# Performance work log

Hardware: AMD Instinct MI355X
Metric: run time of the kernel (lower is better)

The kernel has to match this reference:

```python
import jax, jax.numpy as jnp
import numpy as np

# Fixed production-scale dims (see shape_source)
B, R, WIDTH, T, H, W = 8, 12, 2304, 4, 16, 29
REDUCE, HID, NC, ROI_SP, DEPTH = 1024, 512, 60, 7, 2
SR = 2  # roi_align sampling ratio (fixed; torchvision default -1 is roi-adaptive)


def conv2d(x, w, pad):
    return jax.lax.conv_general_dilated(
        x, w, (1, 1), [(pad, pad), (pad, pad)],
        dimension_numbers=('NCHW', 'OIHW', 'NCHW'))


def maxpool_3x3_s2(x):
    return jax.lax.reduce_window(
        x, -jnp.inf, jax.lax.max, (1, 1, 3, 3), (1, 1, 2, 2),
        [(0, 0), (0, 0), (1, 1), (1, 1)])


def bilinear(img, ys, xs):
    # img [C,h,w]; ys, xs [P] -> [C,P]; matches torchvision bilinear_interpolate
    h, w = img.shape[1], img.shape[2]
    valid = (ys >= -1.0) & (ys <= h) & (xs >= -1.0) & (xs <= w)
    y = jnp.clip(ys, 0.0, h - 1.0)
    x = jnp.clip(xs, 0.0, w - 1.0)
    y0f = jnp.floor(y); x0f = jnp.floor(x)
    iy0 = y0f.astype(jnp.int32); ix0 = x0f.astype(jnp.int32)
    iy1 = jnp.minimum(iy0 + 1, h - 1); ix1 = jnp.minimum(ix0 + 1, w - 1)
    ly = y - y0f; lx = x - x0f; hy = 1.0 - ly; hx = 1.0 - lx
    v00 = img[:, iy0, ix0]; v01 = img[:, iy0, ix1]
    v10 = img[:, iy1, ix0]; v11 = img[:, iy1, ix1]
    out = hy * hx * v00 + hy * lx * v01 + ly * hx * v10 + ly * lx * v11
    return jnp.where(valid[None, :], out, 0.0)


def roi_align_one(img, box):
    # img [C,H,W]; box (x1,y1,x2,y2) in feature coords; aligned=False, scale=1
    x1, y1, x2, y2 = box[0], box[1], box[2], box[3]
    rw = jnp.maximum(x2 - x1, 1.0)
    rh = jnp.maximum(y2 - y1, 1.0)
    bw = rw / ROI_SP; bh = rh / ROI_SP
    g = (jnp.arange(ROI_SP, dtype=jnp.float32)[:, None]
         + (jnp.arange(SR, dtype=jnp.float32)[None, :] + 0.5) / SR).reshape(-1)  # [7*SR]
    ys = y1 + g * bh; xs = x1 + g * bw
    n = ROI_SP * SR
    yy = jnp.repeat(ys, n); xx = jnp.tile(xs, n)
    vals = bilinear(img, yy, xx)                       # [C, n*n]
    vals = vals.reshape(img.shape[0], ROI_SP, SR, ROI_SP, SR)
    return vals.mean(axis=(2, 4))                      # [C,7,7]


def hr2o_layer(x, qw, kw, vw, cw, gamma, beta):
    # x [R, HID, Hp, Wp]; non-local attention across ROIs of one image
    q = conv2d(x, qw, 1)
    k = conv2d(x, kw, 1)
    v = conv2d(x, vw, 1)
    att = jnp.einsum('ichw,jchw->ijhw', q, k) / jnp.sqrt(jnp.float32(HID))
    att = jax.nn.softmax(att, axis=1)                  # softmax over key rois
    virt = jnp.einsum('ijhw,jchw->ichw', att, v)
    mu = virt.mean(axis=(1, 2, 3), keepdims=True)      # GroupNorm(1, HID)
    var = virt.var(axis=(1, 2, 3), keepdims=True)
    virt = (virt - mu) / jnp.sqrt(var + 1e-5)
    virt = virt * gamma[None, :, None, None] + beta[None, :, None, None]
    virt = jax.nn.relu(virt)
    virt = conv2d(virt, cw, 1)                         # mlp_1x1=False -> 3x3 pad 1
    return x + virt                                    # dropout inactive in eval


def setup_inputs() -> dict:
    key = jax.random.key(0)
    ks = jax.random.split(key, 14)
    features = jax.random.normal(ks[0], (B, WIDTH, T, H, W), jnp.float32)
    xy = jax.random.uniform(ks[1], (B, R, 2), minval=0.0, maxval=0.6)
    wh = jax.random.uniform(ks[2], (B, R, 2), minval=0.2, maxval=0.4)
    rois = jnp.concatenate([xy, xy + wh], axis=-1)     # normalized x1,y1,x2,y2

    def w_(k, shape, fan_in):
        return jax.random.normal(k, shape, jnp.float32) * (1.0 / np.sqrt(fan_in))

    return {
        'features': features,
        'rois': rois,
        'conv_reduce_w': w_(ks[3], (REDUCE, WIDTH, 1, 1), WIDTH),
        'conv1_w': w_(ks[4], (HID, 2 * REDUCE, 1, 1), 2 * REDUCE),
        'conv2_w': w_(ks[5], (HID, HID, 3, 3), HID * 9),
        'hr2o_qw': w_(ks[6], (DEPTH, HID, HID, 3, 3), HID * 9),
        'hr2o_kw': w_(ks[7], (DEPTH, HID, HID, 3, 3), HID * 9),
        'hr2o_vw': w_(ks[8], (DEPTH, HID, HID, 3, 3), HID * 9),
        'hr2o_cw': w_(ks[9], (DEPTH, HID, HID, 3, 3), HID * 9),
        'hr2o_gamma': jnp.ones((DEPTH, HID), jnp.float32),
        'hr2o_beta': jnp.zeros((DEPTH, HID), jnp.float32),
        'fc1_w': w_(ks[10], (HID, REDUCE), REDUCE),
        'fc2_w': w_(ks[11], (NC, 2 * HID), 2 * HID),
    }


def reference(features, rois, conv_reduce_w, conv1_w, conv2_w,
              hr2o_qw, hr2o_kw, hr2o_vw, hr2o_cw, hr2o_gamma, hr2o_beta,
              fc1_w, fc2_w):
    feats = features.mean(axis=2)                      # AdaptiveAvgPool3d((1,H,W)) over T
    feats = conv2d(feats, conv_reduce_w, 0)            # [B, REDUCE, H, W]

    scale = jnp.array([W, H, W, H], jnp.float32)
    boxes = rois * scale                               # feature-space coords (detached)
    ra = jax.vmap(lambda img, bxs: jax.vmap(lambda b: roi_align_one(img, b))(bxs))(
        feats, boxes)                                  # [B, R, REDUCE, 7, 7]
    roi_feats = ra.max(axis=(-2, -1)).reshape(B * R, REDUCE)  # MaxPool2d(7)

    # broadcast bg + tiled actor, concat on channels (eff_h=H, eff_w=W)
    bg = jnp.broadcast_to(feats[:, None], (B, R, REDUCE, H, W))
    actor = jnp.broadcast_to(
        roi_feats.reshape(B, R, REDUCE)[..., None, None], (B, R, REDUCE, H, W))
    x = jnp.concatenate([bg, actor], axis=2).reshape(B * R, 2 * REDUCE, H, W)
    x = jax.nn.relu(conv2d(x, conv1_w, 0))             # 1x1
    x = jax.nn.relu(conv2d(x, conv2_w, 0))             # 3x3, Conv2d default pad=0
    x = maxpool_3x3_s2(x)                              # [B*R, HID, 7, 14]
    hp, wp = x.shape[2], x.shape[3]
    x = x.reshape(B, R, HID, hp, wp)
    for d in range(DEPTH):
        x = jax.vmap(lambda xi: hr2o_layer(
            xi, hr2o_qw[d], hr2o_kw[d], hr2o_vw[d], hr2o_cw[d],
            hr2o_gamma[d], hr2o_beta[d]))(x)
    high = x.mean(axis=(-2, -1)).reshape(B * R, HID)   # GAP

    out = jax.nn.relu(roi_feats @ fc1_w.T)
    out = jnp.concatenate([out, high], axis=1)
    return out @ fc2_w.T                               # [B*R, NC]
```

## Files before the change

kernel.cpp:

```cpp
#include <hip/hip_runtime.h>
#include <math.h>

#define BB 8
#define RR 12
#define WIDTH 2304
#define TT 4
#define HH 16
#define WW 29
#define HWIN (HH*WW)
#define REDUCE 1024
#define HID 512
#define NC 60
#define DEPTH 2
#define NIMG (BB*RR)
#define OH2 14
#define OW2 27
#define NSP2 (OH2*OW2)
#define PH 7
#define PW 14
#define NSP (PH*PW)
#define ATT_SCALE 0.044194173824159216f

typedef __attribute__((ext_vector_type(8))) short short8;
typedef __attribute__((ext_vector_type(4))) float floatx4;

__device__ __forceinline__ void split2(float v, unsigned short& h, unsigned short& l)
{
    union { float f; unsigned u; } c; c.f = v;
    unsigned hb = c.u & 0xffff0000u;
    h = (unsigned short)(hb >> 16);
    union { float f; unsigned u; } hc; hc.u = hb;
    float r = v - hc.f;
    union { float f; unsigned u; } rc; rc.f = r;
    unsigned ru = rc.u + 0x7fffu + ((rc.u >> 16) & 1u);
    l = (unsigned short)(ru >> 16);
}

__device__ __forceinline__ void gll16(const void* g, void* l)
{
    __builtin_amdgcn_global_load_lds((const __attribute__((address_space(1))) void*)g,
                                     (__attribute__((address_space(3))) void*)l,
                                     16, 0, 0);
}

#define MFMA3(d, ah_, al_, bh_, bl_) \
    d = __builtin_amdgcn_mfma_f32_16x16x32_bf16(ah_, bh_, d, 0, 0, 0); \
    d = __builtin_amdgcn_mfma_f32_16x16x32_bf16(ah_, bl_, d, 0, 0, 0); \
    d = __builtin_amdgcn_mfma_f32_16x16x32_bf16(al_, bh_, d, 0, 0, 0);

template<int TYPE, int NSEL, bool RELU, bool RESID, int WR, int ZB>
__global__ __launch_bounds__(256, 2)
void tapr_k(const int4* __restrict__ WA0, const int4* __restrict__ WA1, const int4* __restrict__ WA2,
            const ushort* __restrict__ BH, const ushort* __restrict__ BL,
            const float* __restrict__ Res,
            float* __restrict__ Y0, float* __restrict__ Y1, float* __restrict__ Y2)
{
    __shared__ int4 L[2064 + ZB * 8 * WR];
    const int tid = threadIdx.x;
    constexpr int NZP = 96 / ZB;

    int ch, zp, nb = 0;
    if (TYPE == 0) { ch = blockIdx.x / NZP; zp = blockIdx.x % NZP; }
    else { ch = blockIdx.x / (4 * NZP); int r = blockIdx.x % (4 * NZP); nb = r / NZP; zp = r % NZP; }
    int sel = 0, m0;
    if (NSEL == 3) { sel = ch >> 2; m0 = (ch & 3) * 128; }
    else m0 = ch * 128;
    const int z0 = zp * ZB;

    const int4* WA = (NSEL == 3) ? (sel == 0 ? WA0 : sel == 1 ? WA1 : WA2) : WA0;
    float* Y = (NSEL == 3) ? (sel == 0 ? Y0 : sel == 1 ? Y1 : Y2) : Y0;

    const int lane = tid & 63, wv = tid >> 6;
    const int lrow = lane >> 4, lcol = lane & 15;
    constexpr long ALO = 294912;
    constexpr long PLSTR = (TYPE == 1) ? 472L * 512 : 160L * 512;
    const int pbase = (TYPE == 1) ? (((nb * 112) >> 5) * 29 + ((nb * 112) & 31)) : 0;

    int pbnf[7];
#pragma unroll
    for (int nf = 0; nf < 7; ++nf) {
        int col = nf * 16 + lcol;
        if (TYPE == 0) pbnf[nf] = col;
        else { int gn = nb * 112 + col; pbnf[nf] = (gn >> 5) * 29 + (gn & 31) - pbase; }
    }

    int uR[3], uPl[3], uZi[3]; bool uV[3];
    const ushort* uSrc[3];
#pragma unroll
    for (int it = 0; it < 3; ++it) {
        int u = tid + it * 256;
        uV[it] = (u < 2 * ZB * WR);
        int uu = uV[it] ? u : 0;
        uR[it] = uu % WR; uPl[it] = (uu / WR) & 1; uZi[it] = uu / (2 * WR);
        const ushort* P = uPl[it] ? BL : BH;
        uSrc[it] = P + (size_t)(z0 + uZi[it]) * PLSTR + (size_t)(pbase + uR[it]) * 512;
    }

    floatx4 acc[ZB][2][7];
#pragma unroll
    for (int zi = 0; zi < ZB; ++zi)
#pragma unroll
        for (int mf = 0; mf < 2; ++mf)
#pragma unroll
            for (int nf = 0; nf < 7; ++nf) acc[zi][mf][nf] = (floatx4){0.f, 0.f, 0.f, 0.f};

#define BCOPY(CB) { \
    _Pragma("unroll") \
    for (int it = 0; it < 3; ++it) if (uV[it]) { \
        const int4* s = (const int4*)(uSrc[it] + (size_t)(CB) * 32); \
        int4 t0 = s[0], t1 = s[1], t2 = s[2], t3_ = s[3]; \
        int bse = 2064 + uZi[it] * (8 * WR) + uPl[it] * (4 * WR) + uR[it]; \
        L[bse] = t0; L[bse + WR] = t1; L[bse + 2 * WR] = t2; L[bse + 3 * WR] = t3_; \
    } }

#define ASTAGE(KST, BUF) { \
    int k8 = (KST) * 4; \
    _Pragma("unroll") \
    for (int j = 0; j < 4; ++j) { \
        int h = wv * 4 + j, p = h >> 3, g = (h >> 1) & 3, hf = h & 1; \
        gll16(WA + (p ? ALO : 0) + (long)(k8 + g) * 512 + m0 + hf * 64 + lane, \
              L + (BUF) * 1032 + (p * 4 + g) * 129 + hf * 64); \
    } }

#define COMPUTE(BUF, SHV) { \
    const int4* La = L + (BUF) * 1032; \
    short8 ah[2], al[2]; \
    _Pragma("unroll") \
    for (int mf = 0; mf < 2; ++mf) { \
        int au = lrow * 129 + (wv * 2 + mf) * 16 + lcol; \
        ah[mf] = *(const short8*)(La + au); \
        al[mf] = *(const short8*)(La + 516 + au); \
    } \
    _Pragma("unroll") \
    for (int nf = 0; nf < 7; ++nf) { \
        int spl = pbnf[nf] + (SHV); \
        _Pragma("unroll") \
        for (int zi = 0; zi < ZB; ++zi) { \
            const int4* Lb = L + 2064 + zi * (8 * WR) + lrow * WR + spl; \
            short8 bh = *(const short8*)(Lb); \
            short8 bl = *(const short8*)(Lb + 4 * WR); \
            _Pragma("unroll") \
            for (int mf = 0; mf < 2; ++mf) { MFMA3(acc[zi][mf][nf], ah[mf], al[mf], bh, bl) } \
        } \
    } }

    BCOPY(0)
    ASTAGE(0, 0)
    __syncthreads();

    int cur = 0;
    for (int cb = 0; cb < 16; ++cb) {
#pragma unroll
        for (int tap = 0; tap < 9; ++tap) {
            const int kst = cb * 9 + tap;
            const int t3 = tap / 3;
            const int shv = (TYPE == 0) ? (t3 * 16 + (tap - t3 * 3)) : (t3 * 29 + (tap - t3 * 3));
            if (kst < 143) ASTAGE(kst + 1, cur ^ 1)
            COMPUTE(cur, shv)
            __syncthreads();
            cur ^= 1;
        }
        if (cb < 15) {
            BCOPY(cb + 1)
            __syncthreads();
        }
    }

#pragma unroll
    for (int zi = 0; zi < ZB; ++zi) {
        const int z = z0 + zi;
#pragma unroll
        for (int mf = 0; mf < 2; ++mf) {
            int m = m0 + wv * 32 + mf * 16 + lrow * 4;
#pragma unroll
            for (int nf = 0; nf < 7; ++nf) {
                int col = nf * 16 + lcol;
                int sp, realn; bool ok;
                if (TYPE == 0) { int oh = col >> 4, ow = col & 15; ok = ow < 14; sp = oh * 14 + ow; realn = 98; }
                else { int gn = nb * 112 + col; int oh = gn >> 5, ow = gn & 31; ok = ow < 27; sp = oh * 27 + ow; realn = 378; }
                if (ok) {
#pragma unroll
                    for (int r = 0; r < 4; ++r) {
                        size_t idx = ((size_t)z * 512 + m + r) * realn + sp;
                        float v = acc[zi][mf][nf][r];
                        if (RESID) v += Res[idx];
                        if (RELU) v = fmaxf(v, 0.f);
                        Y[idx] = v;
                    }
                }
            }
        }
    }
#undef BCOPY
#undef ASTAGE
#undef COMPUTE
}

template<int KW, int KSTN, int MTOT, long PLSTR, int NREAL>
__global__ __launch_bounds__(256, 2)
void tapc_k(const int4* __restrict__ WA,
            const ushort* __restrict__ BH, const ushort* __restrict__ BL,
            float* __restrict__ Y)
{
    __shared__ int4 L[3872];
    const int tid = threadIdx.x;
    const int z = blockIdx.z, nb = blockIdx.x;
    const int m0 = blockIdx.y * 128;
    const int lane = tid & 63, wv = tid >> 6;
    const int lrow = lane >> 4, lcol = lane & 15;
    constexpr long ALO = (long)KSTN * 4 * MTOT;

    int nU[2], gU[2]; long pbU[2]; bool vU[2];
#pragma unroll
    for (int it = 0; it < 2; ++it) {
        int u = tid + (it << 8);
        vU[it] = (u < 448);
        int uu = vU[it] ? u : 0;
        nU[it] = uu % 112; gU[it] = uu / 112;
        int gn = nb * 112 + nU[it];
        pbU[it] = min(gn, NREAL - 1);
    }
    const ushort* BHz = BH + (size_t)z * PLSTR;
    const ushort* BLz = BL + (size_t)z * PLSTR;

    floatx4 acc[2][7];
#pragma unroll
    for (int mf = 0; mf < 2; ++mf)
#pragma unroll
        for (int nf = 0; nf < 7; ++nf) acc[mf][nf] = (floatx4){0.f, 0.f, 0.f, 0.f};

    short8 rbh[2], rbl[2];

#define STAGE_ISSUE(KST, BUF) { \
    int k8 = (KST) * 4; \
    _Pragma("unroll") \
    for (int j = 0; j < 4; ++j) { \
        int h = wv * 4 + j, p = h >> 3, g = (h >> 1) & 3, hf = h & 1; \
        gll16(WA + (p ? ALO : 0) + (long)(k8 + g) * MTOT + m0 + hf * 64 + lane, \
              L + (BUF) * 1936 + (p * 4 + g) * 129 + hf * 64); \
    } \
    int ci0 = (KST) << 5; \
    _Pragma("unroll") \
    for (int it = 0; it < 2; ++it) if (vU[it]) { \
        size_t o = (size_t)pbU[it] * KW + ci0 + gU[it] * 8; \
        rbh[it] = *(const short8*)(BHz + o); \
        rbl[it] = *(const short8*)(BLz + o); \
    } }

#define STAGE_WRITE(BUF) { \
    _Pragma("unroll") \
    for (int it = 0; it < 2; ++it) if (vU[it]) { \
        *((short8*)(L + (BUF) * 1936 + 1032 + gU[it] * 113 + nU[it])) = rbh[it]; \
        *((short8*)(L + (BUF) * 1936 + 1484 + gU[it] * 113 + nU[it])) = rbl[it]; \
    } }

#define COMPUTE(BUF) { \
    const int4* Lc = L + (BUF) * 1936; \
    short8 ah[2], al[2]; \
    _Pragma("unroll") \
    for (int mf = 0; mf < 2; ++mf) { \
        int au = lrow * 129 + (wv * 2 + mf) * 16 + lcol; \
        ah[mf] = *(const short8*)(Lc + au); \
        al[mf] = *(const short8*)(Lc + 516 + au); \
    } \
    _Pragma("unroll") \
    for (int nf = 0; nf < 7; ++nf) { \
        int bu = 1032 + lrow * 113 + nf * 16 + lcol; \
        short8 bh = *(const short8*)(Lc + bu); \
        short8 bl = *(const short8*)(Lc + bu + 452); \
        _Pragma("unroll") \
        for (int mf = 0; mf < 2; ++mf) { MFMA3(acc[mf][nf], ah[mf], al[mf], bh, bl) } \
    } }

    STAGE_ISSUE(0, 0)
    STAGE_WRITE(0)
    __syncthreads();

    int cur = 0;
    for (int kst = 0; kst < KSTN; ++kst) {
        int nxt = cur ^ 1;
        bool more = (kst + 1 < KSTN);
        if (more) STAGE_ISSUE(kst + 1, nxt)
        COMPUTE(cur)
        if (more) { STAGE_WRITE(nxt) __syncthreads(); }
        cur = nxt;
    }

#pragma unroll
    for (int mf = 0; mf < 2; ++mf) {
        int m = m0 + wv * 32 + mf * 16 + lrow * 4;
#pragma unroll
        for (int nf = 0; nf < 7; ++nf) {
            int col = nf * 16 + lcol;
            int gn = nb * 112 + col;
            if (gn < NREAL) {
#pragma unroll
                for (int r = 0; r < 4; ++r) {
                    size_t idx = ((size_t)z * MTOT + m + r) * NREAL + gn;
                    Y[idx] = acc[mf][nf][r];
                }
            }
        }
    }
#undef STAGE_ISSUE
#undef STAGE_WRITE
#undef COMPUTE
}

__global__ void prep_w_k(const float* __restrict__ s0, const float* __restrict__ s1,
                         const float* __restrict__ s2, const float* __restrict__ s3,
                         int4* __restrict__ dst)
{
    const int c = blockIdx.y;
    const float* src = (c == 0) ? s0 : (c == 1) ? s1 : (c == 2) ? s2 : s3;
    int4* dh = dst + (size_t)c * 589824;
    int4* dl = dh + 294912;
    int idx = blockIdx.x * 256 + threadIdx.x;
    if (idx >= 294912) return;
    int g8 = idx / 512, m = idx & 511;
    unsigned hw[4], lw[4];
#pragma unroll
    for (int j = 0; j < 4; ++j) {
        int k1 = g8 * 8 + 2 * j, k2 = k1 + 1;
        int cb1 = k1 / 288, r1 = k1 % 288, tp1 = r1 >> 5, ci1 = cb1 * 32 + (r1 & 31);
        int cb2 = k2 / 288, r2 = k2 % 288, tp2 = r2 >> 5, ci2 = cb2 * 32 + (r2 & 31);
        float v1 = src[(size_t)m * 4608 + ci1 * 9 + tp1];
        float v2 = src[(size_t)m * 4608 + ci2 * 9 + tp2];
        unsigned short h0, l0, h1, l1;
        split2(v1, h0, l0); split2(v2, h1, l1);
        hw[j] = (unsigned)h0 | ((unsigned)h1 << 16);
        lw[j] = (unsigned)l0 | ((unsigned)l1 << 16);
    }
    dh[idx] = make_int4(hw[0], hw[1], hw[2], hw[3]);
    dl[idx] = make_int4(lw[0], lw[1], lw[2], lw[3]);
}

__global__ void prep_wg_k(const float* __restrict__ src, int ldw, int M, int K8,
                          int4* __restrict__ dst)
{
    int idx = blockIdx.x * 256 + threadIdx.x;
    if (idx >= K8 * M) return;
    int g8 = idx / M, m = idx % M;
    unsigned hw[4], lw[4];
#pragma unroll
    for (int j = 0; j < 4; ++j) {
        int k1 = g8 * 8 + 2 * j;
        float v1 = src[(size_t)m * ldw + k1];
        float v2 = src[(size_t)m * ldw + k1 + 1];
        unsigned short h0, l0, h1, l1;
        split2(v1, h0, l0); split2(v2, h1, l1);
        hw[j] = (unsigned)h0 | ((unsigned)h1 << 16);
        lw[j] = (unsigned)l0 | ((unsigned)l1 << 16);
    }
    dst[idx] = make_int4(hw[0], hw[1], hw[2], hw[3]);
    dst[(size_t)K8 * M + idx] = make_int4(lw[0], lw[1], lw[2], lw[3]);
}

__global__ __launch_bounds__(256)
void tsplit_k(const float* __restrict__ src, ushort* __restrict__ dh, ushort* __restrict__ dl,
              int C, int S, long zsrc, long zdst)
{
    __shared__ float t[64][65];
    const int c0 = blockIdx.x * 64, s0 = blockIdx.y * 64, z = blockIdx.z;
    const float* sz = src + (size_t)z * zsrc;
    const int tx = threadIdx.x & 63, ty = threadIdx.x >> 6;
#pragma unroll
    for (int i = 0; i < 16; ++i) {
        int cc = i * 4 + ty;
        int c = c0 + cc, s = s0 + tx;
        t[cc][tx] = (c < C && s < S) ? sz[(size_t)c * S + s] : 0.f;
    }
    __syncthreads();
#pragma unroll
    for (int i = 0; i < 16; ++i) {
        int ss = i * 4 + ty;
        int s = s0 + ss, c = c0 + tx;
        if (s < S && c < C) {
            unsigned short h, l;
            split2(t[tx][ss], h, l);
            size_t o = (size_t)z * zdst + (size_t)s * C + c;
            dh[o] = h; dl[o] = l;
        }
    }
}

__global__ __launch_bounds__(256)
void tsplit_c2_k(const float* __restrict__ bg, const float* __restrict__ bias1,
                 ushort* __restrict__ dh, ushort* __restrict__ dl)
{
    __shared__ float t[64][65];
    const int c0 = blockIdx.x * 64, s0 = blockIdx.y * 64, z = blockIdx.z;
    const int b = z / RR;
    const int tx = threadIdx.x & 63, ty = threadIdx.x >> 6;
#pragma unroll
    for (int i = 0; i < 16; ++i) {
        int cc = i * 4 + ty;
        int s = s0 + tx;
        t[cc][tx] = (s < 464) ? bg[((size_t)b * 512 + c0 + cc) * 464 + s] : 0.f;
    }
    __syncthreads();
    const float bv = bias1[z * 512 + c0 + tx];
#pragma unroll
    for (int i = 0; i < 16; ++i) {
        int ss = i * 4 + ty;
        int s = s0 + ss, c = c0 + tx;
        if (s < 472) {
            float v = (s < 464) ? fmaxf(t[tx][ss] + bv, 0.f) : 0.f;
            unsigned short h, l;
            split2(v, h, l);
            size_t o = (size_t)z * 241664 + (size_t)s * 512 + c;
            dh[o] = h; dl[o] = l;
        }
    }
}

__global__ __launch_bounds__(256)
void tsplit_pad_k(const float* __restrict__ x, ushort* __restrict__ dh, ushort* __restrict__ dl)
{
    __shared__ float t[64 * 99];
    const int c0 = blockIdx.x * 64, z = blockIdx.y;
    const int tid = threadIdx.x;
#pragma unroll
    for (int i = 0; i < 25; ++i) {
        int idx = tid + i * 256;
        if (idx < 6272) {
            int c = idx / 98, s = idx % 98;
            t[c * 99 + s] = x[((size_t)z * 512 + c0 + c) * 98 + s];
        }
    }
    __syncthreads();
#pragma unroll
    for (int i = 0; i < 40; ++i) {
        int idx = tid + i * 256;
        int sp = idx >> 6, c = idx & 63;
        int r = sp >> 4, col = sp & 15;
        float v = (r >= 1 && r <= 7 && col >= 1 && col <= 14) ? t[c * 99 + (r - 1) * 14 + col - 1] : 0.f;
        unsigned short h, l;
        split2(v, h, l);
        size_t o = (size_t)z * 81920 + (size_t)sp * 512 + c0 + c;
        dh[o] = h; dl[o] = l;
    }
}

__global__ void tmean_k(const float* __restrict__ f, float* __restrict__ o, int total)
{
    int i = blockIdx.x * blockDim.x + threadIdx.x;
    if (i >= total) return;
    int p = i % HWIN; long bc = i / HWIN;
    const float* src = f + bc * (long)TT * HWIN + p;
    o[i] = (src[0] + src[HWIN] + src[2 * HWIN] + src[3 * HWIN]) * 0.25f;
}

__global__ __launch_bounds__(256)
void roi_align_k(const float* __restrict__ feats, const float* __restrict__ rois,
                 float* __restrict__ roi_feats)
{
    __shared__ int s_o00[196], s_o01[196], s_o10[196], s_o11[196];
    __shared__ float s_w[4][196];
    const int n = blockIdx.x;
    const int b = n / RR;
    const int t = threadIdx.x;
    if (t < 196) {
        float x1 = rois[n * 4 + 0] * WW, y1 = rois[n * 4 + 1] * HH;
        float x2 = rois[n * 4 + 2] * WW, y2 = rois[n * 4 + 3] * HH;
        float rw = fmaxf(x2 - x1, 1.f), rh = fmaxf(y2 - y1, 1.f);
        float bw = rw / 7.f, bh = rh / 7.f;
        int j = t / 14, i = t % 14;
        float gy = (float)(j >> 1) + ((j & 1) + 0.5f) * 0.5f;
        float gx = (float)(i >> 1) + ((i & 1) + 0.5f) * 0.5f;
        float ys = y1 + gy * bh, xs = x1 + gx * bw;
        bool valid = (ys >= -1.f) && (ys <= (float)HH) && (xs >= -1.f) && (xs <= (float)WW);
        float y = fminf(fmaxf(ys, 0.f), (float)(HH - 1));
        float x = fminf(fmaxf(xs, 0.f), (float)(WW - 1));
        float y0f = floorf(y), x0f = floorf(x);
        int iy0 = (int)y0f, ix0 = (int)x0f;
        int iy1 = min(iy0 + 1, HH - 1), ix1 = min(ix0 + 1, WW - 1);
        float ly = y - y0f, lx = x - x0f, hy = 1.f - ly, hx = 1.f - lx;
        float msk = valid ? 1.f : 0.f;
        s_o00[t] = iy0 * WW + ix0; s_o01[t] = iy0 * WW + ix1;
        s_o10[t] = iy1 * WW + ix0; s_o11[t] = iy1 * WW + ix1;
        s_w[0][t] = hy * hx * msk; s_w[1][t] = hy * lx * msk;
        s_w[2][t] = ly * hx * msk; s_w[3][t] = ly * lx * msk;
    }
    __syncthreads();
    for (int c = t; c < REDUCE; c += 256) {
        const float* img = feats + ((long)(b * REDUCE + c)) * HWIN;
        float mx = -INFINITY;
        for (int bin = 0; bin < 49; ++bin) {
            int by_ = bin / 7, bx = bin % 7;
            float s = 0.f;
#pragma unroll
            for (int sy = 0; sy < 2; ++sy)
#pragma unroll
                for (int sx = 0; sx < 2; ++sx) {
                    int ss = (by_ * 2 + sy) * 14 + bx * 2 + sx;
                    s += s_w[0][ss] * img[s_o00[ss]] + s_w[1][ss] * img[s_o01[ss]]
                       + s_w[2][ss] * img[s_o10[ss]] + s_w[3][ss] * img[s_o11[ss]];
                }
            mx = fmaxf(mx, s * 0.25f);
        }
        roi_feats[(long)n * REDUCE + c] = mx;
    }
}

__global__ void dots_k(const float* __restrict__ Xr, const float* __restrict__ Wt,
                       int ldw, int woff, float* __restrict__ Y,
                       int Nrows, int M, int K, int relu)
{
    int idx = blockIdx.x * blockDim.x + threadIdx.x;
    if (idx >= Nrows * M) return;
    int o = idx / Nrows, n = idx % Nrows;
    const float* xr = Xr + (long)n * K;
    const float* w = Wt + (long)o * ldw + woff;
    float acc = 0.f;
    for (int k = 0; k < K; ++k) acc = fmaf(xr[k], w[k], acc);
    if (relu) acc = fmaxf(acc, 0.f);
    Y[(long)n * M + o] = acc;
}

__global__ void maxpool_k(const float* __restrict__ in, float* __restrict__ out, int total)
{
    int idx = blockIdx.x * blockDim.x + threadIdx.x;
    if (idx >= total) return;
    int ow = idx % PW; int r = idx / PW; int oh = r % PH; long nc = r / PH;
    const float* src = in + nc * NSP2;
    float m = -INFINITY;
    for (int kh = 0; kh < 3; ++kh) {
        int ih = oh * 2 - 1 + kh; if (ih < 0 || ih >= OH2) continue;
        for (int kw = 0; kw < 3; ++kw) {
            int iw = ow * 2 - 1 + kw; if (iw < 0 || iw >= OW2) continue;
            m = fmaxf(m, src[ih * OW2 + iw]);
        }
    }
    out[idx] = m;
}

__global__ __launch_bounds__(256)
void att2_k(const float* __restrict__ q, const float* __restrict__ k, float* __restrict__ att)
{
    __shared__ float qs[5376];
    __shared__ float ks[5376];
    __shared__ float sc[1008];
    const int b = blockIdx.x, p0 = blockIdx.y * 7;
    const int tid = threadIdx.x;

    int itI[4], itJ[4], itP[4]; bool itV[4];
#pragma unroll
    for (int r = 0; r < 4; ++r) {
        int item = tid + (r << 8);
        itV[r] = item < 1008;
        int it = itV[r] ? item : 0;
        int ij = it / 7; itP[r] = it % 7;
        itI[r] = ij / 12; itJ[r] = ij % 12;
    }
    float acc[4] = {0.f, 0.f, 0.f, 0.f};

    for (int cc0 = 0; cc0 < 512; cc0 += 64) {
        for (int l = tid; l < 5376; l += 256) {
            int i = l / 448, r = l % 448, c = r / 7, p = r % 7;
            size_t off = ((size_t)(b * 12 + i) * 512 + cc0 + c) * 98 + p0 + p;
            qs[l] = q[off];
            ks[l] = k[off];
        }
        __syncthreads();
#pragma unroll
        for (int r = 0; r < 4; ++r) {
            if (itV[r]) {
                const float* qp = qs + itI[r] * 448 + itP[r];
                const float* kp = ks + itJ[r] * 448 + itP[r];
                float a = acc[r];
#pragma unroll 8
                for (int c = 0; c < 64; ++c) a = fmaf(qp[c * 7], kp[c * 7], a);
                acc[r] = a;
            }
        }
        __syncthreads();
    }
#pragma unroll
    for (int r = 0; r < 4; ++r)
        if (itV[r]) sc[tid + (r << 8)] = acc[r] * ATT_SCALE;
    __syncthreads();
    if (tid < 84) {
        int i = tid / 7, p = tid % 7;
        float m = -INFINITY;
        float v[12];
#pragma unroll
        for (int j = 0; j < 12; ++j) { v[j] = sc[(i * 12 + j) * 7 + p]; m = fmaxf(m, v[j]); }
        float s = 0.f;
#pragma unroll
        for (int j = 0; j < 12; ++j) { v[j] = expf(v[j] - m); s += v[j]; }
        float inv = 1.f / s;
#pragma unroll
        for (int j = 0; j < 12; ++j)
            att[((size_t)(b * 12 + i) * 12 + j) * 98 + p0 + p] = v[j] * inv;
    }
}

__global__ __launch_bounds__(256)
void virt2_k(const float* __restrict__ att, const float* __restrict__ v, float* __restrict__ virt)
{
    __shared__ float as_[14112];
    const int b = blockIdx.x, cb = blockIdx.y;
    const int tid = threadIdx.x;
    for (int l = tid; l < 14112; l += 256) as_[l] = att[(size_t)b * 14112 + l];
    __syncthreads();

    for (int it = tid; it < 6272; it += 256) {
        int c = cb * 64 + it / 98, p = it % 98;
        float o[12];
#pragma unroll
        for (int i = 0; i < 12; ++i) o[i] = 0.f;
#pragma unroll
        for (int j = 0; j < 12; ++j) {
            float vj = v[((size_t)(b * 12 + j) * 512 + c) * 98 + p];
#pragma unroll
            for (int i = 0; i < 12; ++i) o[i] = fmaf(as_[(i * 12 + j) * 98 + p], vj, o[i]);
        }
#pragma unroll
        for (int i = 0; i < 12; ++i)
            virt[((size_t)(b * 12 + i) * 512 + c) * 98 + p] = o[i];
    }
}

__global__ __launch_bounds__(256)
void stats_k(const float* __restrict__ virt, float* __restrict__ mu, float* __restrict__ rstd)
{
    int n = blockIdx.x;
    const float* src = virt + (long)n * HID * NSP;
    float s = 0.f, q = 0.f;
    for (int i = threadIdx.x; i < HID * NSP; i += 256) {
        float v = src[i]; s += v; q = fmaf(v, v, q);
    }
    for (int off = 32; off; off >>= 1) { s += __shfl_down(s, off); q += __shfl_down(q, off); }
    __shared__ float ss[4], sq[4];
    int w = threadIdx.x >> 6;
    if ((threadIdx.x & 63) == 0) { ss[w] = s; sq[w] = q; }
    __syncthreads();
    if (threadIdx.x == 0) {
        float S = ss[0] + ss[1] + ss[2] + ss[3];
        float Q = sq[0] + sq[1] + sq[2] + sq[3];
        const float invN = 1.f / (HID * NSP);
        float m = S * invN;
        float var = Q * invN - m * m;
        mu[n] = m; rstd[n] = rsqrtf(var + 1e-5f);
    }
}

__global__ void norm_k(float* __restrict__ virt, const float* __restrict__ mu,
                       const float* __restrict__ rstd,
                       const float* __restrict__ gamma, const float* __restrict__ beta)
{
    int idx = blockIdx.x * blockDim.x + threadIdx.x;
    const int TOT = NIMG * HID * NSP;
    if (idx >= TOT) return;
    int n = idx / (HID * NSP);
    int c = (idx / NSP) % HID;
    float val = (virt[idx] - mu[n]) * rstd[n] * gamma[c] + beta[c];
    virt[idx] = fmaxf(val, 0.f);
}

__global__ void meanpool_k(const float* __restrict__ x, float* __restrict__ high)
{
    int idx = blockIdx.x * blockDim.x + threadIdx.x;
    if (idx >= NIMG * HID) return;
    const float* src = x + (long)idx * NSP;
    float s = 0.f;
    for (int p = 0; p < NSP; ++p) s += src[p];
    high[idx] = s * (1.f / NSP);
}

__global__ void final_k(const float* __restrict__ fc1o, const float* __restrict__ high,
                        const float* __restrict__ fc2, float* __restrict__ out)
{
    int idx = blockIdx.x * blockDim.x + threadIdx.x;
    if (idx >= NIMG * NC) return;
    int n = idx / NC, o = idx % NC;
    const float* w = fc2 + (long)o * (2 * HID);
    const float* a = fc1o + (long)n * HID;
    const float* h = high + (long)n * HID;
    float acc = 0.f;
    for (int c = 0; c < HID; ++c) acc = fmaf(a[c], w[c], acc);
    for (int c = 0; c < HID; ++c) acc = fmaf(h[c], w[HID + c], acc);
    out[idx] = acc;
}

extern "C" void kernel_launch(void* const* d_in, const int* in_sizes, int n_in,
                              void* d_out, int out_size, void* d_ws, size_t ws_size,
                              hipStream_t stream)
{
    (void)in_sizes; (void)n_in; (void)out_size; (void)ws_size;
    const float* features = (const float*)d_in[0];
    const float* rois     = (const float*)d_in[1];
    const float* w_reduce = (const float*)d_in[2];
    const float* w_conv1  = (const float*)d_in[3];
    const float* w_conv2  = (const float*)d_in[4];
    const float* qw       = (const float*)d_in[5];
    const float* kw       = (const float*)d_in[6];
    const float* vw       = (const float*)d_in[7];
    const float* cw       = (const float*)d_in[8];
    const float* gamma    = (const float*)d_in[9];
    const float* beta     = (const float*)d_in[10];
    const float* fc1      = (const float*)d_in[11];
    const float* fc2      = (const float*)d_in[12];
    float* ws = (float*)d_ws;

    float*  tmean = ws + 0;
    ushort* tmTH  = (ushort*)(ws + 8552448);
    ushort* tmTL  = (ushort*)(ws + 12828672);
    float*  feats = ws + 17104896;
    ushort* ftTH  = (ushort*)(ws + 0);
    ushort* ftTL  = (ushort*)(ws + 1900544);
    ushort* B2H   = (ushort*)(ws + 0);
    ushort* B2L   = (ushort*)(ws + 11599872);
    int4*   WTQ   = (int4*)(ws + 0);
    float*  bg    = ws + 23199744;
    float*  out2  = ws + 23199744;
    float*  qb    = ws + 23199744;
    float*  kb    = ws + 28016640;
    float*  vb    = ws + 32833536;
    ushort* PTH   = (ushort*)(ws + 41779200);
    ushort* PTL   = (ushort*)(ws + 45711360);
    float*  xb    = ws + 49643520;
    float*  virt  = ws + 54460416;
    int4*   WTS   = (int4*)(ws + 59277312);
    float*  rf    = ws + 61636608;
    float*  bias1 = ws + 61734912;
    float*  fc1o  = ws + 61784064;
    float*  attb  = ws + 61833216;
    float*  mu    = ws + 61946112;
    float*  rstd  = ws + 61946240;
    float*  high  = ws + 61946368;

    dim3 blk(256);

    prep_wg_k<<<1152, blk, 0, stream>>>(w_reduce, 2304, 1024, 288, WTS);

    { int tot = BB * WIDTH * HWIN;
      tmean_k<<<(tot + 255) / 256, blk, 0, stream>>>(features, tmean, tot); }

    tsplit_k<<<dim3(36, 8, 8), blk, 0, stream>>>(tmean, tmTH, tmTL, 2304, 464, 1069056, 1069056);

    tapc_k<2304, 72, 1024, 464L * 2304, 464>
        <<<dim3(5, 8, 8), blk, 0, stream>>>(WTS, tmTH, tmTL, feats);

    tsplit_k<<<dim3(16, 8, 8), blk, 0, stream>>>(feats, ftTH, ftTL, 1024, 464, 475136, 475136);

    roi_align_k<<<96, blk, 0, stream>>>(feats, rois, rf);
    dots_k<<<(NIMG * HID + 255) / 256, blk, 0, stream>>>(rf, w_conv1, 2048, 1024, bias1, NIMG, HID, REDUCE, 0);
    dots_k<<<(NIMG * HID + 255) / 256, blk, 0, stream>>>(rf, fc1, 1024, 0, fc1o, NIMG, HID, REDUCE, 1);

    prep_wg_k<<<256, blk, 0, stream>>>(w_conv1, 2048, 512, 128, WTS);
    tapc_k<1024, 32, 512, 464L * 1024, 464>
        <<<dim3(5, 4, 8), blk, 0, stream>>>(WTS, ftTH, ftTL, bg);

    prep_w_k<<<dim3(1152, 1), blk, 0, stream>>>(w_conv2, w_conv2, w_conv2, w_conv2, WTS);
    tsplit_c2_k<<<dim3(8, 8, 96), blk, 0, stream>>>(bg, bias1, B2H, B2L);

    tapr_k<1, 1, true, false, 165, 2><<<768, blk, 0, stream>>>(
        WTS, nullptr, nullptr, B2H, B2L, nullptr, out2, nullptr, nullptr);

    { int tot = NIMG * HID * NSP;
      maxpool_k<<<(tot + 255) / 256, blk, 0, stream>>>(out2, xb, tot); }

    for (int d = 0; d < DEPTH; ++d) {
        long woff = (long)d * HID * HID * 9;
        prep_w_k<<<dim3(1152, 4), blk, 0, stream>>>(qw + woff, kw + woff, vw + woff, cw + woff, WTQ);

        tsplit_pad_k<<<dim3(8, 96), blk, 0, stream>>>(xb, PTH, PTL);
        tapr_k<0, 3, false, false, 161, 2><<<576, blk, 0, stream>>>(
            WTQ, WTQ + 589824, WTQ + 2 * 589824, PTH, PTL, nullptr, qb, kb, vb);

        att2_k<<<dim3(8, 14), blk, 0, stream>>>(qb, kb, attb);
        virt2_k<<<dim3(8, 8), blk, 0, stream>>>(attb, vb, virt);
        stats_k<<<96, blk, 0, stream>>>(virt, mu, rstd);
        { int tot = NIMG * HID * NSP;
          norm_k<<<(tot + 255) / 256, blk, 0, stream>>>(virt, mu, rstd, gamma + d * HID, beta + d * HID); }

        tsplit_pad_k<<<dim3(8, 96), blk, 0, stream>>>(virt, PTH, PTL);
        tapr_k<0, 1, false, true, 161, 1><<<384, blk, 0, stream>>>(
            WTQ + 3 * 589824, nullptr, nullptr, PTH, PTL, xb, xb, nullptr, nullptr);
    }

    meanpool_k<<<(NIMG * HID + 255) / 256, blk, 0, stream>>>(xb, high);
    final_k<<<(NIMG * NC + 255) / 256, blk, 0, stream>>>(fc1o, high, fc2, (float*)d_out);
}
```

Before: 2.980 ms.

## Load weight fragments directly into registers and drop per-tap LDS staging

The 3x3 tap-conv kernel now reads its A (weight) fragments straight from global memory into double-buffered registers, replacing the async global-to-LDS staging with a double-buffered LDS area. This removes the per-tap __syncthreads and the LDS traffic for weights, leaving a barrier only around B-tile refills. In exchange it adds register pressure and relies on cache hits for uncoalesced-ish direct global loads, with less latency hiding than the previous LDS pipeline.

```diff
diff --git a/kernel.cpp b/kernel.cpp
--- a/kernel.cpp
+++ b/kernel.cpp
@@ -50,12 +50,12 @@
 
 template<int TYPE, int NSEL, bool RELU, bool RESID, int WR, int ZB>
 __global__ __launch_bounds__(256, 2)
-void tapr_k(const int4* __restrict__ WA0, const int4* __restrict__ WA1, const int4* __restrict__ WA2,
-            const ushort* __restrict__ BH, const ushort* __restrict__ BL,
-            const float* __restrict__ Res,
-            float* __restrict__ Y0, float* __restrict__ Y1, float* __restrict__ Y2)
-{
-    __shared__ int4 L[2064 + ZB * 8 * WR];
+void tapr3_k(const int4* __restrict__ WA0, const int4* __restrict__ WA1, const int4* __restrict__ WA2,
+             const ushort* __restrict__ BH, const ushort* __restrict__ BL,
+             const float* __restrict__ Res,
+             float* __restrict__ Y0, float* __restrict__ Y1, float* __restrict__ Y2)
+{
+    __shared__ int4 L[ZB * 8 * WR];
     const int tid = threadIdx.x;
     constexpr int NZP = 96 / ZB;
 
@@ -96,6 +96,8 @@
         uSrc[it] = P + (size_t)(z0 + uZi[it]) * PLSTR + (size_t)(pbase + uR[it]) * 512;
     }
 
+    const long abase0 = (long)lrow * 512 + m0 + wv * 32 + lcol;
+
     floatx4 acc[ZB][2][7];
 #pragma unroll
     for (int zi = 0; zi < ZB; ++zi)
@@ -103,67 +105,60 @@
         for (int mf = 0; mf < 2; ++mf)
 #pragma unroll
             for (int nf = 0; nf < 7; ++nf) acc[zi][mf][nf] = (floatx4){0.f, 0.f, 0.f, 0.f};
+
+    short8 ah[2][2], al[2][2];
+
+#define ALOAD(KST, S) { \
+    long ab = (long)(KST) * 2048 + abase0; \
+    _Pragma("unroll") \
+    for (int mf = 0; mf < 2; ++mf) { \
+        ah[S][mf] = *(const short8*)(WA + ab + mf * 16); \
+        al[S][mf] = *(const short8*)(WA + ALO + ab + mf * 16); \
+    } }
 
 #define BCOPY(CB) { \
     _Pragma("unroll") \
     for (int it = 0; it < 3; ++it) if (uV[it]) { \
         const int4* s = (const int4*)(uSrc[it] + (size_t)(CB) * 32); \
         int4 t0 = s[0], t1 = s[1], t2 = s[2], t3_ = s[3]; \
-        int bse = 2064 + uZi[it] * (8 * WR) + uPl[it] * (4 * WR) + uR[it]; \
+        int bse = uZi[it] * (8 * WR) + uPl[it] * (4 * WR) + uR[it]; \
         L[bse] = t0; L[bse + WR] = t1; L[bse + 2 * WR] = t2; L[bse + 3 * WR] = t3_; \
     } }
 
-#define ASTAGE(KST, BUF) { \
-    int k8 = (KST) * 4; \
-    _Pragma("unroll") \
-    for (int j = 0; j < 4; ++j) { \
-        int h = wv * 4 + j, p = h >> 3, g = (h >> 1) & 3, hf = h & 1; \
-        gll16(WA + (p ? ALO : 0) + (long)(k8 + g) * 512 + m0 + hf * 64 + lane, \
-              L + (BUF) * 1032 + (p * 4 + g) * 129 + hf * 64); \
-    } }
-
-#define COMPUTE(BUF, SHV) { \
-    const int4* La = L + (BUF) * 1032; \
-    short8 ah[2], al[2]; \
-    _Pragma("unroll") \
-    for (int mf = 0; mf < 2; ++mf) { \
-        int au = lrow * 129 + (wv * 2 + mf) * 16 + lcol; \
-        ah[mf] = *(const short8*)(La + au); \
-        al[mf] = *(const short8*)(La + 516 + au); \
-    } \
+#define COMPUTE(S, SHV) { \
     _Pragma("unroll") \
     for (int nf = 0; nf < 7; ++nf) { \
         int spl = pbnf[nf] + (SHV); \
         _Pragma("unroll") \
         for (int zi = 0; zi < ZB; ++zi) { \
-            const int4* Lb = L + 2064 + zi * (8 * WR) + lrow * WR + spl; \
+            const int4* Lb = L + zi * (8 * WR) + lrow * WR + spl; \
             short8 bh = *(const short8*)(Lb); \
             short8 bl = *(const short8*)(Lb + 4 * WR); \
             _Pragma("unroll") \
-            for (int mf = 0; mf < 2; ++mf) { MFMA3(acc[zi][mf][nf], ah[mf], al[mf], bh, bl) } \
+            for (int mf = 0; mf < 2; ++mf) { MFMA3(acc[zi][mf][nf], ah[S][mf], al[S][mf], bh, bl) } \
         } \
     } }
 
     BCOPY(0)
-    ASTAGE(0, 0)
-    __syncthreads();
-
-    int cur = 0;
+    __syncthreads();
+    ALOAD(0, 0)
+
     for (int cb = 0; cb < 16; ++cb) {
 #pragma unroll
         for (int tap = 0; tap < 9; ++tap) {
-            const int kst = cb * 9 + tap;
+            const int kst9 = cb * 9 + tap;
             const int t3 = tap / 3;
             const int shv = (TYPE == 0) ? (t3 * 16 + (tap - t3 * 3)) : (t3 * 29 + (tap - t3 * 3));
-            if (kst < 143) ASTAGE(kst + 1, cur ^ 1)
-            COMPUTE(cur, shv)
+            if (kst9 < 143) ALOAD(kst9 + 1, ((tap + 1) & 1))
+            COMPUTE((tap & 1), shv)
+        }
+        if (cb < 15) {
             __syncthreads();
-            cur ^= 1;
-        }
-        if (cb < 15) {
             BCOPY(cb + 1)
             __syncthreads();
         }
+#pragma unroll
+        for (int mf = 0; mf < 2; ++mf) { ah[0][mf] = ah[1][mf]; al[0][mf] = al[1][mf]; }
     }
 
 #pragma unroll
@@ -191,8 +186,8 @@
             }
         }
     }
+#undef ALOAD
 #undef BCOPY
-#undef ASTAGE
 #undef COMPUTE
 }
 
@@ -756,7 +751,7 @@
     prep_w_k<<<dim3(1152, 1), blk, 0, stream>>>(w_conv2, w_conv2, w_conv2, w_conv2, WTS);
     tsplit_c2_k<<<dim3(8, 8, 96), blk, 0, stream>>>(bg, bias1, B2H, B2L);
 
-    tapr_k<1, 1, true, false, 165, 2><<<768, blk, 0, stream>>>(
+    tapr3_k<1, 1, true, false, 165, 2><<<768, blk, 0, stream>>>(
         WTS, nullptr, nullptr, B2H, B2L, nullptr, out2, nullptr, nullptr);
 
     { int tot = NIMG * HID * NSP;
@@ -767,7 +762,7 @@
         prep_w_k<<<dim3(1152, 4), blk, 0, stream>>>(qw + woff, kw + woff, vw + woff, cw + woff, WTQ);
 
         tsplit_pad_k<<<dim3(8, 96), blk, 0, stream>>>(xb, PTH, PTL);
-        tapr_k<0, 3, false, false, 161, 2><<<576, blk, 0, stream>>>(
+        tapr3_k<0, 3, false, false, 161, 2><<<576, blk, 0, stream>>>(
             WTQ, WTQ + 589824, WTQ + 2 * 589824, PTH, PTL, nullptr, qb, kb, vb);
 
         att2_k<<<dim3(8, 14), blk, 0, stream>>>(qb, kb, attb);
@@ -777,7 +772,7 @@
           norm_k<<<(tot + 255) / 256, blk, 0, stream>>>(virt, mu, rstd, gamma + d * HID, beta + d * HID); }
 
         tsplit_pad_k<<<dim3(8, 96), blk, 0, stream>>>(virt, PTH, PTL);
-        tapr_k<0, 1, false, true, 161, 1><<<384, blk, 0, stream>>>(
+        tapr3_k<0, 1, false, true, 161, 1><<<384, blk, 0, stream>>>(
             WTQ + 3 * 589824, nullptr, nullptr, PTH, PTL, xb, xb, nullptr, nullptr);
     }
 
```

Result: slower. 5.817 ms (+95.2%).

## Split-K the HR2O output conv across two blocks and merge partials

Applied to the files above, without the earlier changes.

Adds a split-K template parameter to the tap conv kernel so the final hr2o 3x3 conv splits its 16 channel blocks into two halves. This doubles the grid from 384 to 768 blocks so more CUs stay busy. Each half writes partial sums into the q/k scratch buffers, and a new elementwise merge kernel adds both to the residual. The cost is an extra launch plus extra global traffic for the partials and the merge pass.

```diff
diff --git a/kernel.cpp b/kernel.cpp
--- a/kernel.cpp
+++ b/kernel.cpp
@@ -48,7 +48,7 @@
     d = __builtin_amdgcn_mfma_f32_16x16x32_bf16(ah_, bl_, d, 0, 0, 0); \
     d = __builtin_amdgcn_mfma_f32_16x16x32_bf16(al_, bh_, d, 0, 0, 0);
 
-template<int TYPE, int NSEL, bool RELU, bool RESID, int WR, int ZB>
+template<int TYPE, int NSEL, bool RELU, bool RESID, int WR, int ZB, int KSP>
 __global__ __launch_bounds__(256, 2)
 void tapr_k(const int4* __restrict__ WA0, const int4* __restrict__ WA1, const int4* __restrict__ WA2,
             const ushort* __restrict__ BH, const ushort* __restrict__ BL,
@@ -59,16 +59,24 @@
     const int tid = threadIdx.x;
     constexpr int NZP = 96 / ZB;
 
-    int ch, zp, nb = 0;
-    if (TYPE == 0) { ch = blockIdx.x / NZP; zp = blockIdx.x % NZP; }
-    else { ch = blockIdx.x / (4 * NZP); int r = blockIdx.x % (4 * NZP); nb = r / NZP; zp = r % NZP; }
+    int ch, zp, nb = 0, kh = 0;
+    if (TYPE == 0) {
+        int b = blockIdx.x;
+        if (KSP == 2) { kh = b / (4 * NZP); b %= (4 * NZP); }
+        ch = b / NZP; zp = b % NZP;
+    } else {
+        ch = blockIdx.x / (4 * NZP); int r = blockIdx.x % (4 * NZP); nb = r / NZP; zp = r % NZP;
+    }
     int sel = 0, m0;
     if (NSEL == 3) { sel = ch >> 2; m0 = (ch & 3) * 128; }
     else m0 = ch * 128;
     const int z0 = zp * ZB;
+    const int cb0 = (KSP == 2) ? kh * 8 : 0;
+    const int cb1 = (KSP == 2) ? cb0 + 8 : 16;
 
     const int4* WA = (NSEL == 3) ? (sel == 0 ? WA0 : sel == 1 ? WA1 : WA2) : WA0;
-    float* Y = (NSEL == 3) ? (sel == 0 ? Y0 : sel == 1 ? Y1 : Y2) : Y0;
+    float* Y = (KSP == 2) ? (kh == 0 ? Y0 : Y1)
+             : ((NSEL == 3) ? (sel == 0 ? Y0 : sel == 1 ? Y1 : Y2) : Y0);
 
     const int lane = tid & 63, wv = tid >> 6;
     const int lrow = lane >> 4, lcol = lane & 15;
@@ -144,23 +152,23 @@
         } \
     } }
 
-    BCOPY(0)
-    ASTAGE(0, 0)
+    BCOPY(cb0)
+    ASTAGE(cb0 * 9, 0)
     __syncthreads();
 
     int cur = 0;
-    for (int cb = 0; cb < 16; ++cb) {
+    for (int cb = cb0; cb < cb1; ++cb) {
 #pragma unroll
         for (int tap = 0; tap < 9; ++tap) {
             const int kst = cb * 9 + tap;
             const int t3 = tap / 3;
             const int shv = (TYPE == 0) ? (t3 * 16 + (tap - t3 * 3)) : (t3 * 29 + (tap - t3 * 3));
-            if (kst < 143) ASTAGE(kst + 1, cur ^ 1)
+            if (kst < cb1 * 9 - 1) ASTAGE(kst + 1, cur ^ 1)
             COMPUTE(cur, shv)
             __syncthreads();
             cur ^= 1;
         }
-        if (cb < 15) {
+        if (cb < cb1 - 1) {
             BCOPY(cb + 1)
             __syncthreads();
         }
@@ -194,6 +202,14 @@
 #undef BCOPY
 #undef ASTAGE
 #undef COMPUTE
+}
+
+__global__ void merge_k(float* __restrict__ xb, const float* __restrict__ p0,
+                        const float* __restrict__ p1, int total)
+{
+    int idx = blockIdx.x * blockDim.x + threadIdx.x;
+    if (idx >= total) return;
+    xb[idx] = xb[idx] + (p0[idx] + p1[idx]);
 }
 
 template<int KW, int KSTN, int MTOT, long PLSTR, int NREAL>
@@ -756,7 +772,7 @@
     prep_w_k<<<dim3(1152, 1), blk, 0, stream>>>(w_conv2, w_conv2, w_conv2, w_conv2, WTS);
     tsplit_c2_k<<<dim3(8, 8, 96), blk, 0, stream>>>(bg, bias1, B2H, B2L);
 
-    tapr_k<1, 1, true, false, 165, 2><<<768, blk, 0, stream>>>(
+    tapr_k<1, 1, true, false, 165, 2, 1><<<768, blk, 0, stream>>>(
         WTS, nullptr, nullptr, B2H, B2L, nullptr, out2, nullptr, nullptr);
 
     { int tot = NIMG * HID * NSP;
@@ -767,7 +783,7 @@
         prep_w_k<<<dim3(1152, 4), blk, 0, stream>>>(qw + woff, kw + woff, vw + woff, cw + woff, WTQ);
 
         tsplit_pad_k<<<dim3(8, 96), blk, 0, stream>>>(xb, PTH, PTL);
-        tapr_k<0, 3, false, false, 161, 2><<<576, blk, 0, stream>>>(
+        tapr_k<0, 3, false, false, 161, 2, 1><<<576, blk, 0, stream>>>(
             WTQ, WTQ + 589824, WTQ + 2 * 589824, PTH, PTL, nullptr, qb, kb, vb);
 
         att2_k<<<dim3(8, 14), blk, 0, stream>>>(qb, kb, attb);
@@ -777,8 +793,10 @@
           norm_k<<<(tot + 255) / 256, blk, 0, stream>>>(virt, mu, rstd, gamma + d * HID, beta + d * HID); }
 
         tsplit_pad_k<<<dim3(8, 96), blk, 0, stream>>>(virt, PTH, PTL);
-        tapr_k<0, 1, false, true, 161, 1><<<384, blk, 0, stream>>>(
-            WTQ + 3 * 589824, nullptr, nullptr, PTH, PTL, xb, xb, nullptr, nullptr);
+        tapr_k<0, 1, false, false, 161, 1, 2><<<768, blk, 0, stream>>>(
+            WTQ + 3 * 589824, nullptr, nullptr, PTH, PTL, nullptr, qb, kb, nullptr);
+        { int tot = NIMG * HID * NSP;
+          merge_k<<<(tot + 255) / 256, blk, 0, stream>>>(xb, qb, kb, tot); }
     }
 
     meanpool_k<<<(NIMG * HID + 255) / 256, blk, 0, stream>>>(xb, high);
```

New measurement: 2.939 ms (median of 2 runs). Within noise of the previous version (-1.4%).
